# Optimization experiments

Hardware: AMD Instinct MI355X
Metric: run time of the kernel (lower is better)

## Reference

```python
import jax, jax.numpy as jnp
import numpy as np

B, S, E = 8, 2048, 256
NQ = 10
FF = 1024


def _cnot(state, c, t, n):
    # state: [T, 2^n]; wire 0 is the most-significant bit.
    T = state.shape[0]
    s = state.reshape((T,) + (2,) * n)
    ctrl0 = jnp.take(s, 0, axis=c + 1)
    ctrl1 = jnp.take(s, 1, axis=c + 1)
    # target axis index after removing the control axis
    t_ax = t + 1 if (t + 1) < (c + 1) else t
    ctrl1 = jnp.flip(ctrl1, axis=t_ax)  # X on target where control==1
    s = jnp.stack([ctrl0, ctrl1], axis=c + 1)
    return s.reshape(T, -1)


def _quantum_layer(tok, theta, n):
    # tok: [T, E] real; uses first n features as RX angles. Returns [T, n] PauliZ expvals.
    T = tok.shape[0]
    half = tok[:, :n] * 0.5
    c = jnp.cos(half).astype(jnp.complex64)
    s = (-1j * jnp.sin(half)).astype(jnp.complex64)
    # RX(theta)|0> = cos(t/2)|0> - i sin(t/2)|1>; build product state wire-by-wire
    state = jnp.ones((T, 1), dtype=jnp.complex64)
    for w in range(n):
        qb = jnp.stack([c[:, w], s[:, w]], axis=1)  # [T, 2]
        state = (state[:, :, None] * qb[:, None, :]).reshape(T, -1)
    # trainable RY per wire
    th = theta * 0.5
    for w in range(n):
        ct, st = jnp.cos(th[w]), jnp.sin(th[w])
        U = jnp.stack([jnp.stack([ct, -st]), jnp.stack([st, ct])]).astype(jnp.complex64)
        sr = state.reshape(T, 2 ** w, 2, -1)
        state = jnp.einsum('ij,tajb->taib', U, sr).reshape(T, -1)
    # CNOT ring
    for cw in range(n - 1):
        state = _cnot(state, cw, cw + 1, n)
    state = _cnot(state, n - 1, 0, n)
    probs = state.real ** 2 + state.imag ** 2  # [T, 2^n]
    idx = jnp.arange(2 ** n)
    bits = (idx[None, :] >> (n - 1 - jnp.arange(n)[:, None])) & 1  # [n, 2^n]
    z = (1.0 - 2.0 * bits).astype(probs.dtype)
    return probs @ z.T  # [T, n]


def setup_inputs() -> dict:
    key = jax.random.key(0)
    ks = jax.random.split(key, 6)
    return {
        'x': jax.random.normal(ks[0], (B, S, E), dtype=jnp.float32),
        'theta': jax.random.normal(ks[1], (NQ,), dtype=jnp.float32),
        'w1': jax.random.normal(ks[2], (FF, NQ), dtype=jnp.float32) * (1.0 / np.sqrt(NQ)),
        'b1': jax.random.normal(ks[3], (FF,), dtype=jnp.float32) * 0.02,
        'w2': jax.random.normal(ks[4], (E, FF), dtype=jnp.float32) * (1.0 / np.sqrt(FF)),
        'b2': jax.random.normal(ks[5], (E,), dtype=jnp.float32) * 0.02,
    }


def reference(x, theta, w1, b1, w2, b2):
    b, s, e = x.shape
    n = theta.shape[0]
    q = _quantum_layer(x.reshape(b * s, e), theta, n).reshape(b, s, n)
    # dropout is identity in eval mode
    h = jax.nn.relu(q @ w1.T + b1)
    return h @ w2.T + b2
```

## Files before the change

### kernel.cpp

```cpp
#include <hip/hip_runtime.h>
#include <hip/hip_bf16.h>
#include <math.h>

typedef __attribute__((ext_vector_type(8))) short bf16x8;
typedef __attribute__((ext_vector_type(4))) float f32x4;

#define T_TOT 16384
#define E_ 256
#define FF_ 1024
#define NQ 10
#define TB 64
#define CH 256
#define NCHUNK (FF_ / CH)
#define HGRAN (TB * CH)

__device__ __forceinline__ unsigned pkbf(float a, float b) {
    __hip_bfloat162 t = __float22bfloat162_rn(make_float2(a, b));
    return *(unsigned*)&t;
}

__global__ __launch_bounds__(256) void ffq_prep(
    const float* __restrict__ w2, const float* __restrict__ w1,
    uint4* __restrict__ w2f, uint4* __restrict__ w1f)
{
    int id = blockIdx.x * 256 + threadIdx.x;
    if (id < 32768) {
        int n  = id >> 7;
        int k0 = (id & 127) * 8;
        const float4* s = (const float4*)(w2 + (size_t)n * FF_ + k0);
        float4 a = s[0], b = s[1];
        uint4 v;
        v.x = pkbf(a.x, a.y);
        v.y = pkbf(a.z, a.w);
        v.z = pkbf(b.x, b.y);
        v.w = pkbf(b.z, b.w);
        int idx = ((k0 >> 5) * 16 + (n >> 4)) * 64 + ((k0 >> 3) & 3) * 16 + (n & 15);
        w2f[idx] = v;
    } else if (id < 32768 + 4096) {
        int id2 = id - 32768;
        int l = id2 & 63, nt = id2 >> 6;
        int n = nt * 16 + (l & 15);
        int g = l >> 4;
        float o[8];
#pragma unroll
        for (int j = 0; j < 8; ++j) {
            int k = g * 8 + j;
            o[j] = (k < NQ) ? w1[n * NQ + k] : 0.f;
        }
        uint4 v;
        v.x = pkbf(o[0], o[1]);
        v.y = pkbf(o[2], o[3]);
        v.z = pkbf(o[4], o[5]);
        v.w = pkbf(o[6], o[7]);
        w1f[id2] = v;
    }
}

__global__ __launch_bounds__(512, 4) void ffq_mfma(
    const float* __restrict__ x, const float* __restrict__ theta,
    const float* __restrict__ b1, const float* __restrict__ b2,
    const bf16x8* __restrict__ w1f, const bf16x8* __restrict__ w2f,
    float* __restrict__ out)
{
    __shared__ unsigned short q_s[4 * 64 * 8];
    __shared__ unsigned short hs[2 * HGRAN];

    const int tid  = threadIdx.x;
    const int l    = tid & 63;
    const int wv   = tid >> 6;
    const int lr   = l & 15;
    const int g    = l >> 4;
    const int wk   = wv >> 2;
    const int wc   = wv & 3;
    const int chb  = blockIdx.x & 1;
    const int tb   = (blockIdx.x >> 1) * TB;
    const int nc0  = chb * 8 + wc * 2;
    const int nc1  = nc0 + 1;

    if (tid < TB) {
        const int t = tb + tid;
        float xv[NQ];
        {
            float4 a = *(const float4*)(x + (size_t)t * E_);
            float4 b = *(const float4*)(x + (size_t)t * E_ + 4);
            float2 c = *(const float2*)(x + (size_t)t * E_ + 8);
            xv[0]=a.x; xv[1]=a.y; xv[2]=a.z; xv[3]=a.w;
            xv[4]=b.x; xv[5]=b.y; xv[6]=b.z; xv[7]=b.w;
            xv[8]=c.x; xv[9]=c.y;
        }
        float mm[NQ];
#pragma unroll
        for (int w = 0; w < NQ; ++w) mm[w] = cosf(theta[w]) * cosf(xv[w]);
        float qv[NQ];
        {
            float p = mm[0];
#pragma unroll
            for (int w = 1; w < NQ; ++w) { p *= mm[w]; qv[w] = p; }
            float p0 = mm[1];
#pragma unroll
            for (int w = 2; w < NQ; ++w) p0 *= mm[w];
            qv[0] = p0;
        }
        uint4 s0, s1;
        s0.x = pkbf(qv[0], qv[1]);
        s0.y = pkbf(qv[2], qv[3]);
        s0.z = pkbf(qv[4], qv[5]);
        s0.w = pkbf(qv[6], qv[7]);
        s1.x = pkbf(qv[8], qv[9]);
        s1.y = 0; s1.z = 0; s1.w = 0;
        int tt = tid >> 4, r = tid & 15;
        uint4* base = (uint4*)q_s + tt * 64;
        base[r]      = s0;
        base[16 + r] = s1;
        base[32 + r] = make_uint4(0, 0, 0, 0);
        base[48 + r] = make_uint4(0, 0, 0, 0);
    }
    __syncthreads();

    f32x4 acc[4][2];
#pragma unroll
    for (int tt = 0; tt < 4; ++tt)
#pragma unroll
        for (int nn = 0; nn < 2; ++nn) acc[tt][nn] = (f32x4){0.f,0.f,0.f,0.f};

#define H_PHASE(cc, hdst)                                                      \
    {                                                                          \
        bf16x8 wfa = w1f[((cc) * 16 + wv * 2 + 0) * 64 + l];                   \
        bf16x8 wfb = w1f[((cc) * 16 + wv * 2 + 1) * 64 + l];                   \
        float4 bba = *(const float4*)(b1 + ((cc) * 16 + wv * 2 + 0) * 16 + g * 4); \
        float4 bbb = *(const float4*)(b1 + ((cc) * 16 + wv * 2 + 1) * 16 + g * 4); \
        bf16x8 qfr[4];                                                         \
        _Pragma("unroll")                                                      \
        for (int tt = 0; tt < 4; ++tt)                                         \
            qfr[tt] = ((const bf16x8*)q_s)[tt * 64 + l];                       \
        _Pragma("unroll")                                                      \
        for (int fi = 0; fi < 2; ++fi) {                                       \
            const int ftl = wv * 2 + fi;                                       \
            bf16x8 wf = fi ? wfb : wfa;                                        \
            float4 bb = fi ? bbb : bba;                                        \
            const int fl   = ftl * 16 + g * 4;                                 \
            const int sl   = (fl & 31) >> 3;                                   \
            const int gran = (fl >> 5) * 64 + lr + 16 * sl;                    \
            _Pragma("unroll")                                                  \
            for (int tt = 0; tt < 4; ++tt) {                                   \
                f32x4 d = {0.f, 0.f, 0.f, 0.f};                                \
                d = __builtin_amdgcn_mfma_f32_16x16x32_bf16(                   \
                        wf, qfr[tt], d, 0, 0, 0);                              \
                unsigned p0 = pkbf(fmaxf(d[0] + bb.x, 0.f),                    \
                                   fmaxf(d[1] + bb.y, 0.f));                   \
                unsigned p1 = pkbf(fmaxf(d[2] + bb.z, 0.f),                    \
                                   fmaxf(d[3] + bb.w, 0.f));                   \
                unsigned byteoff = (unsigned)(tt * 512 + gran) * 16u           \
                                 + (unsigned)(fl & 7) * 2u;                    \
                *(uint2*)((char*)(hdst) + byteoff) = make_uint2(p0, p1);       \
            }                                                                  \
        }                                                                      \
    }

#define OUT_STEP(J)                                                            \
    {                                                                          \
        const int kk  = c * 8 + wk * 4 + (J);                                  \
        const int kkn = ((J) < 3) ? kk + 1 : ((c < NCHUNK - 1) ? kk + 5 : kk); \
        bf16x8 af[4];                                                          \
        _Pragma("unroll")                                                      \
        for (int tt = 0; tt < 4; ++tt)                                         \
            af[tt] = hc[(tt * 8 + wk * 4 + (J)) * 64 + l];                     \
        bf16x8 bn0 = w2f[(kkn * 16 + nc0) * 64 + l];                           \
        bf16x8 bn1 = w2f[(kkn * 16 + nc1) * 64 + l];                           \
        _Pragma("unroll")                                                      \
        for (int tt = 0; tt < 4; ++tt)                                         \
            acc[tt][0] = __builtin_amdgcn_mfma_f32_16x16x32_bf16(              \
                af[tt], bc0, acc[tt][0], 0, 0, 0);                             \
        _Pragma("unroll")                                                      \
        for (int tt = 0; tt < 4; ++tt)                                         \
            acc[tt][1] = __builtin_amdgcn_mfma_f32_16x16x32_bf16(              \
                af[tt], bc1, acc[tt][1], 0, 0, 0);                             \
        bc0 = bn0; bc1 = bn1;                                                  \
    }

    H_PHASE(0, hs)
    bf16x8 bc0 = w2f[((wk * 4) * 16 + nc0) * 64 + l];
    bf16x8 bc1 = w2f[((wk * 4) * 16 + nc1) * 64 + l];
    __syncthreads();

    for (int c = 0; c < NCHUNK; ++c) {
        const bf16x8*   hc = (const bf16x8*)(hs + (c & 1) * HGRAN);
        unsigned short* hn = hs + ((c & 1) ^ 1) * HGRAN;

        __builtin_amdgcn_s_setprio(1);
        OUT_STEP(0)
        OUT_STEP(1)
        OUT_STEP(2)
        OUT_STEP(3)
        __builtin_amdgcn_s_setprio(0);

        if (c < NCHUNK - 1) {
            H_PHASE(c + 1, hn)
        }
        __syncthreads();
    }
#undef OUT_STEP
#undef H_PHASE

    float* pbuf = (float*)hs;
    const int idx = wc * 64 + l;
    if (wk == 1) {
#pragma unroll
        for (int tt = 0; tt < 4; ++tt) {
            *(f32x4*)&pbuf[idx * 36 + tt * 8]     = acc[tt][0];
            *(f32x4*)&pbuf[idx * 36 + tt * 8 + 4] = acc[tt][1];
        }
    }
    __syncthreads();
    if (wk == 0) {
#pragma unroll
        for (int tt = 0; tt < 4; ++tt) {
            f32x4 p0 = *(const f32x4*)&pbuf[idx * 36 + tt * 8];
            f32x4 p1 = *(const f32x4*)&pbuf[idx * 36 + tt * 8 + 4];
#pragma unroll
            for (int r = 0; r < 4; ++r) { acc[tt][0][r] += p0[r]; acc[tt][1][r] += p1[r]; }
        }

#pragma unroll
        for (int nn = 0; nn < 2; ++nn) {
            const int col = (nc0 + nn) * 16 + lr;
            const float bbv = b2[col];
#pragma unroll
            for (int tt = 0; tt < 4; ++tt) {
#pragma unroll
                for (int r = 0; r < 4; ++r) {
                    int tr = tb + tt * 16 + g * 4 + r;
                    out[(size_t)tr * E_ + col] = acc[tt][nn][r] + bbv;
                }
            }
        }
    }
}

extern "C" void kernel_launch(void* const* d_in, const int* in_sizes, int n_in,
                              void* d_out, int out_size, void* d_ws, size_t ws_size,
                              hipStream_t stream) {
    const float* x     = (const float*)d_in[0];
    const float* theta = (const float*)d_in[1];
    const float* w1    = (const float*)d_in[2];
    const float* b1    = (const float*)d_in[3];
    const float* w2    = (const float*)d_in[4];
    const float* b2    = (const float*)d_in[5];
    float* out = (float*)d_out;

    uint4* w2f = (uint4*)d_ws;
    uint4* w1f = (uint4*)((char*)d_ws + 512 * 1024);

    hipLaunchKernelGGL(ffq_prep, dim3(144), dim3(256), 0, stream,
                       w2, w1, w2f, w1f);
    hipLaunchKernelGGL(ffq_mfma, dim3(2 * T_TOT / TB), dim3(512), 0, stream,
                       x, theta, b1, b2,
                       (const bf16x8*)w1f, (const bf16x8*)w2f, out);
}
```

Before: 26.20 us.

## Fuse weight bf16 conversion into main kernel, drop separate prep launch

```diff
diff --git a/kernel.cpp b/kernel.cpp
--- a/kernel.cpp
+++ b/kernel.cpp
@@ -18,48 +18,17 @@
     __hip_bfloat162 t = __float22bfloat162_rn(make_float2(a, b));
     return *(unsigned*)&t;
 }
-
-__global__ __launch_bounds__(256) void ffq_prep(
-    const float* __restrict__ w2, const float* __restrict__ w1,
-    uint4* __restrict__ w2f, uint4* __restrict__ w1f)
-{
-    int id = blockIdx.x * 256 + threadIdx.x;
-    if (id < 32768) {
-        int n  = id >> 7;
-        int k0 = (id & 127) * 8;
-        const float4* s = (const float4*)(w2 + (size_t)n * FF_ + k0);
-        float4 a = s[0], b = s[1];
-        uint4 v;
-        v.x = pkbf(a.x, a.y);
-        v.y = pkbf(a.z, a.w);
-        v.z = pkbf(b.x, b.y);
-        v.w = pkbf(b.z, b.w);
-        int idx = ((k0 >> 5) * 16 + (n >> 4)) * 64 + ((k0 >> 3) & 3) * 16 + (n & 15);
-        w2f[idx] = v;
-    } else if (id < 32768 + 4096) {
-        int id2 = id - 32768;
-        int l = id2 & 63, nt = id2 >> 6;
-        int n = nt * 16 + (l & 15);
-        int g = l >> 4;
-        float o[8];
-#pragma unroll
-        for (int j = 0; j < 8; ++j) {
-            int k = g * 8 + j;
-            o[j] = (k < NQ) ? w1[n * NQ + k] : 0.f;
-        }
-        uint4 v;
-        v.x = pkbf(o[0], o[1]);
-        v.y = pkbf(o[2], o[3]);
-        v.z = pkbf(o[4], o[5]);
-        v.w = pkbf(o[6], o[7]);
-        w1f[id2] = v;
-    }
-}
-
-__global__ __launch_bounds__(512, 4) void ffq_mfma(
+__device__ __forceinline__ bf16x8 cvt8(float4 a, float4 b) {
+    uint4 v;
+    v.x = pkbf(a.x, a.y); v.y = pkbf(a.z, a.w);
+    v.z = pkbf(b.x, b.y); v.w = pkbf(b.z, b.w);
+    return __builtin_bit_cast(bf16x8, v);
+}
+
+__global__ __launch_bounds__(512, 4) void ffq_fused(
     const float* __restrict__ x, const float* __restrict__ theta,
-    const float* __restrict__ b1, const float* __restrict__ b2,
-    const bf16x8* __restrict__ w1f, const bf16x8* __restrict__ w2f,
+    const float* __restrict__ w1, const float* __restrict__ b1,
+    const float* __restrict__ w2, const float* __restrict__ b2,
     float* __restrict__ out)
 {
     __shared__ unsigned short q_s[4 * 64 * 8];
@@ -76,6 +45,9 @@
     const int tb   = (blockIdx.x >> 1) * TB;
     const int nc0  = chb * 8 + wc * 2;
     const int nc1  = nc0 + 1;
+
+    const float* w2p0 = w2 + (size_t)(nc0 * 16 + lr) * FF_ + g * 8;
+    const float* w2p1 = w2 + (size_t)(nc1 * 16 + lr) * FF_ + g * 8;
 
     if (tid < TB) {
         const int t = tb + tid;
@@ -125,8 +97,25 @@
 
 #define H_PHASE(cc, hdst)                                                      \
     {                                                                          \
-        bf16x8 wfa = w1f[((cc) * 16 + wv * 2 + 0) * 64 + l];                   \
-        bf16x8 wfb = w1f[((cc) * 16 + wv * 2 + 1) * 64 + l];                   \
+        bf16x8 wfv[2];                                                         \
+        _Pragma("unroll")                                                      \
+        for (int fi = 0; fi < 2; ++fi) {                                       \
+            const int ntg = (cc) * 16 + wv * 2 + fi;                           \
+            const float* row = w1 + (size_t)(ntg * 16 + lr) * NQ;              \
+            float4 wa = {0.f,0.f,0.f,0.f}, wb = {0.f,0.f,0.f,0.f};             \
+            if (g == 0) {                                                      \
+                float2 p0 = *(const float2*)(row + 0);                         \
+                float2 p1 = *(const float2*)(row + 2);                         \
+                float2 p2 = *(const float2*)(row + 4);                         \
+                float2 p3 = *(const float2*)(row + 6);                         \
+                wa = make_float4(p0.x, p0.y, p1.x, p1.y);                      \
+                wb = make_float4(p2.x, p2.y, p3.x, p3.y);                      \
+            } else if (g == 1) {                                               \
+                float2 p0 = *(const float2*)(row + 8);                         \
+                wa.x = p0.x; wa.y = p0.y;                                      \
+            }                                                                  \
+            wfv[fi] = cvt8(wa, wb);                                            \
+        }                                                                      \
         float4 bba = *(const float4*)(b1 + ((cc) * 16 + wv * 2 + 0) * 16 + g * 4); \
         float4 bbb = *(const float4*)(b1 + ((cc) * 16 + wv * 2 + 1) * 16 + g * 4); \
         bf16x8 qfr[4];                                                         \
@@ -136,7 +125,6 @@
         _Pragma("unroll")                                                      \
         for (int fi = 0; fi < 2; ++fi) {                                       \
             const int ftl = wv * 2 + fi;                                       \
-            bf16x8 wf = fi ? wfb : wfa;                                        \
             float4 bb = fi ? bbb : bba;                                        \
             const int fl   = ftl * 16 + g * 4;                                 \
             const int sl   = (fl & 31) >> 3;                                   \
@@ -145,7 +133,7 @@
             for (int tt = 0; tt < 4; ++tt) {                                   \
                 f32x4 d = {0.f, 0.f, 0.f, 0.f};                                \
                 d = __builtin_amdgcn_mfma_f32_16x16x32_bf16(                   \
-                        wf, qfr[tt], d, 0, 0, 0);                              \
+                        wfv[fi], qfr[tt], d, 0, 0, 0);                         \
                 unsigned p0 = pkbf(fmaxf(d[0] + bb.x, 0.f),                    \
                                    fmaxf(d[1] + bb.y, 0.f));                   \
                 unsigned p1 = pkbf(fmaxf(d[2] + bb.z, 0.f),                    \
@@ -161,12 +149,16 @@
     {                                                                          \
         const int kk  = c * 8 + wk * 4 + (J);                                  \
         const int kkn = ((J) < 3) ? kk + 1 : ((c < NCHUNK - 1) ? kk + 5 : kk); \
+        bf16x8 bc0 = cvt8(br0a, br0b);                                         \
+        bf16x8 bc1 = cvt8(br1a, br1b);                                         \
+        br0a = *(const float4*)(w2p0 + kkn * 32);                              \
+        br0b = *(const float4*)(w2p0 + kkn * 32 + 4);                          \
+        br1a = *(const float4*)(w2p1 + kkn * 32);                              \
+        br1b = *(const float4*)(w2p1 + kkn * 32 + 4);                          \
         bf16x8 af[4];                                                          \
         _Pragma("unroll")                                                      \
         for (int tt = 0; tt < 4; ++tt)                                         \
             af[tt] = hc[(tt * 8 + wk * 4 + (J)) * 64 + l];                     \
-        bf16x8 bn0 = w2f[(kkn * 16 + nc0) * 64 + l];                           \
-        bf16x8 bn1 = w2f[(kkn * 16 + nc1) * 64 + l];                           \
         _Pragma("unroll")                                                      \
         for (int tt = 0; tt < 4; ++tt)                                         \
             acc[tt][0] = __builtin_amdgcn_mfma_f32_16x16x32_bf16(              \
@@ -175,12 +167,13 @@
         for (int tt = 0; tt < 4; ++tt)                                         \
             acc[tt][1] = __builtin_amdgcn_mfma_f32_16x16x32_bf16(              \
                 af[tt], bc1, acc[tt][1], 0, 0, 0);                             \
-        bc0 = bn0; bc1 = bn1;                                                  \
     }
 
     H_PHASE(0, hs)
-    bf16x8 bc0 = w2f[((wk * 4) * 16 + nc0) * 64 + l];
-    bf16x8 bc1 = w2f[((wk * 4) * 16 + nc1) * 64 + l];
+    float4 br0a = *(const float4*)(w2p0 + (wk * 4) * 32);
+    float4 br0b = *(const float4*)(w2p0 + (wk * 4) * 32 + 4);
+    float4 br1a = *(const float4*)(w2p1 + (wk * 4) * 32);
+    float4 br1b = *(const float4*)(w2p1 + (wk * 4) * 32 + 4);
     __syncthreads();
 
     for (int c = 0; c < NCHUNK; ++c) {
@@ -248,12 +241,6 @@
     const float* b2    = (const float*)d_in[5];
     float* out = (float*)d_out;
 
-    uint4* w2f = (uint4*)d_ws;
-    uint4* w1f = (uint4*)((char*)d_ws + 512 * 1024);
-
-    hipLaunchKernelGGL(ffq_prep, dim3(144), dim3(256), 0, stream,
-                       w2, w1, w2f, w1f);
-    hipLaunchKernelGGL(ffq_mfma, dim3(2 * T_TOT / TB), dim3(512), 0, stream,
-                       x, theta, b1, b2,
-                       (const bf16x8*)w1f, (const bf16x8*)w2f, out);
-}
+    hipLaunchKernelGGL(ffq_fused, dim3(2 * T_TOT / TB), dim3(512), 0, stream,
+                       x, theta, w1, b1, w2, b2, out);
+}
```

Result: slower. 43.81 us (+67.2%).

## Double token tile per block with 1024 threads and halve FF chunk size

Applied to the files above, without the earlier changes.

```diff
diff --git a/kernel.cpp b/kernel.cpp
--- a/kernel.cpp
+++ b/kernel.cpp
@@ -9,8 +9,8 @@
 #define E_ 256
 #define FF_ 1024
 #define NQ 10
-#define TB 64
-#define CH 256
+#define TB 128
+#define CH 128
 #define NCHUNK (FF_ / CH)
 #define HGRAN (TB * CH)
 
@@ -56,13 +56,13 @@
     }
 }
 
-__global__ __launch_bounds__(512, 4) void ffq_mfma(
+__global__ __launch_bounds__(1024, 4) void ffq_mfma(
     const float* __restrict__ x, const float* __restrict__ theta,
     const float* __restrict__ b1, const float* __restrict__ b2,
     const bf16x8* __restrict__ w1f, const bf16x8* __restrict__ w2f,
     float* __restrict__ out)
 {
-    __shared__ unsigned short q_s[4 * 64 * 8];
+    __shared__ unsigned short q_s[8 * 64 * 8];
     __shared__ unsigned short hs[2 * HGRAN];
 
     const int tid  = threadIdx.x;
@@ -70,8 +70,10 @@
     const int wv   = tid >> 6;
     const int lr   = l & 15;
     const int g    = l >> 4;
-    const int wk   = wv >> 2;
+    const int tg   = wv >> 3;
+    const int wk   = (wv >> 2) & 1;
     const int wc   = wv & 3;
+    const int ftl  = wv & 7;
     const int chb  = blockIdx.x & 1;
     const int tb   = (blockIdx.x >> 1) * TB;
     const int nc0  = chb * 8 + wc * 2;
@@ -123,114 +125,115 @@
 #pragma unroll
         for (int nn = 0; nn < 2; ++nn) acc[tt][nn] = (f32x4){0.f,0.f,0.f,0.f};
 
-#define H_PHASE(cc, hdst)                                                      \
+#define H_PHASE(hdst, WF, BBC)                                                 \
     {                                                                          \
-        bf16x8 wfa = w1f[((cc) * 16 + wv * 2 + 0) * 64 + l];                   \
-        bf16x8 wfb = w1f[((cc) * 16 + wv * 2 + 1) * 64 + l];                   \
-        float4 bba = *(const float4*)(b1 + ((cc) * 16 + wv * 2 + 0) * 16 + g * 4); \
-        float4 bbb = *(const float4*)(b1 + ((cc) * 16 + wv * 2 + 1) * 16 + g * 4); \
         bf16x8 qfr[4];                                                         \
         _Pragma("unroll")                                                      \
-        for (int tt = 0; tt < 4; ++tt)                                         \
-            qfr[tt] = ((const bf16x8*)q_s)[tt * 64 + l];                       \
-        _Pragma("unroll")                                                      \
-        for (int fi = 0; fi < 2; ++fi) {                                       \
-            const int ftl = wv * 2 + fi;                                       \
-            bf16x8 wf = fi ? wfb : wfa;                                        \
-            float4 bb = fi ? bbb : bba;                                        \
-            const int fl   = ftl * 16 + g * 4;                                 \
-            const int sl   = (fl & 31) >> 3;                                   \
-            const int gran = (fl >> 5) * 64 + lr + 16 * sl;                    \
-            _Pragma("unroll")                                                  \
-            for (int tt = 0; tt < 4; ++tt) {                                   \
-                f32x4 d = {0.f, 0.f, 0.f, 0.f};                                \
-                d = __builtin_amdgcn_mfma_f32_16x16x32_bf16(                   \
-                        wf, qfr[tt], d, 0, 0, 0);                              \
-                unsigned p0 = pkbf(fmaxf(d[0] + bb.x, 0.f),                    \
-                                   fmaxf(d[1] + bb.y, 0.f));                   \
-                unsigned p1 = pkbf(fmaxf(d[2] + bb.z, 0.f),                    \
-                                   fmaxf(d[3] + bb.w, 0.f));                   \
-                unsigned byteoff = (unsigned)(tt * 512 + gran) * 16u           \
-                                 + (unsigned)(fl & 7) * 2u;                    \
-                *(uint2*)((char*)(hdst) + byteoff) = make_uint2(p0, p1);       \
-            }                                                                  \
+        for (int j = 0; j < 4; ++j)                                            \
+            qfr[j] = ((const bf16x8*)q_s)[(tg * 4 + j) * 64 + l];              \
+        const int fl   = ftl * 16 + g * 4;                                     \
+        const int kkl  = fl >> 5;                                              \
+        const int sl   = (fl & 31) >> 3;                                       \
+        const int gran = kkl * 64 + lr + 16 * sl;                              \
+        _Pragma("unroll")                                                      \
+        for (int j = 0; j < 4; ++j) {                                          \
+            const int tt = tg * 4 + j;                                         \
+            f32x4 d = __builtin_amdgcn_mfma_f32_16x16x32_bf16(                 \
+                    (WF), qfr[j], (BBC), 0, 0, 0);                             \
+            unsigned p0 = pkbf(fmaxf(d[0], 0.f), fmaxf(d[1], 0.f));            \
+            unsigned p1 = pkbf(fmaxf(d[2], 0.f), fmaxf(d[3], 0.f));            \
+            unsigned byteoff = (unsigned)(tt * 256 + gran) * 16u               \
+                             + (unsigned)(fl & 7) * 2u;                        \
+            *(uint2*)((char*)(hdst) + byteoff) = make_uint2(p0, p1);           \
         }                                                                      \
     }
 
 #define OUT_STEP(J)                                                            \
     {                                                                          \
-        const int kk  = c * 8 + wk * 4 + (J);                                  \
-        const int kkn = ((J) < 3) ? kk + 1 : ((c < NCHUNK - 1) ? kk + 5 : kk); \
-        bf16x8 af[4];                                                          \
-        _Pragma("unroll")                                                      \
-        for (int tt = 0; tt < 4; ++tt)                                         \
-            af[tt] = hc[(tt * 8 + wk * 4 + (J)) * 64 + l];                     \
+        const int kk  = c * 4 + wk * 2 + (J);                                  \
+        const int kkn = ((J) == 0) ? kk + 1                                    \
+                      : ((c < NCHUNK - 1) ? kk + 3 : kk);                      \
         bf16x8 bn0 = w2f[(kkn * 16 + nc0) * 64 + l];                           \
         bf16x8 bn1 = w2f[(kkn * 16 + nc1) * 64 + l];                           \
-        _Pragma("unroll")                                                      \
-        for (int tt = 0; tt < 4; ++tt)                                         \
-            acc[tt][0] = __builtin_amdgcn_mfma_f32_16x16x32_bf16(              \
-                af[tt], bc0, acc[tt][0], 0, 0, 0);                             \
-        _Pragma("unroll")                                                      \
-        for (int tt = 0; tt < 4; ++tt)                                         \
-            acc[tt][1] = __builtin_amdgcn_mfma_f32_16x16x32_bf16(              \
-                af[tt], bc1, acc[tt][1], 0, 0, 0);                             \
+        bf16x8 af[4];                                                          \
+        _Pragma("unroll")                                                      \
+        for (int j = 0; j < 4; ++j)                                            \
+            af[j] = hc[((tg * 4 + j) * 4 + wk * 2 + (J)) * 64 + l];            \
+        _Pragma("unroll")                                                      \
+        for (int j = 0; j < 4; ++j)                                            \
+            acc[j][0] = __builtin_amdgcn_mfma_f32_16x16x32_bf16(               \
+                af[j], bc0, acc[j][0], 0, 0, 0);                               \
+        _Pragma("unroll")                                                      \
+        for (int j = 0; j < 4; ++j)                                            \
+            acc[j][1] = __builtin_amdgcn_mfma_f32_16x16x32_bf16(               \
+                af[j], bc1, acc[j][1], 0, 0, 0);                               \
         bc0 = bn0; bc1 = bn1;                                                  \
     }
 
-    H_PHASE(0, hs)
-    bf16x8 bc0 = w2f[((wk * 4) * 16 + nc0) * 64 + l];
-    bf16x8 bc1 = w2f[((wk * 4) * 16 + nc1) * 64 + l];
+    bf16x8 wfc = w1f[(0 * 8 + ftl) * 64 + l];
+    f32x4  bbc = *(const f32x4*)(b1 + (0 * 8 + ftl) * 16 + g * 4);
+    H_PHASE(hs, wfc, bbc)
+    bf16x8 bc0 = w2f[((wk * 2) * 16 + nc0) * 64 + l];
+    bf16x8 bc1 = w2f[((wk * 2) * 16 + nc1) * 64 + l];
     __syncthreads();
 
     for (int c = 0; c < NCHUNK; ++c) {
         const bf16x8*   hc = (const bf16x8*)(hs + (c & 1) * HGRAN);
         unsigned short* hn = hs + ((c & 1) ^ 1) * HGRAN;
 
+        if (c < NCHUNK - 1) {
+            wfc = w1f[((c + 1) * 8 + ftl) * 64 + l];
+            bbc = *(const f32x4*)(b1 + ((c + 1) * 8 + ftl) * 16 + g * 4);
+        }
+
         __builtin_amdgcn_s_setprio(1);
         OUT_STEP(0)
         OUT_STEP(1)
-        OUT_STEP(2)
-        OUT_STEP(3)
         __builtin_amdgcn_s_setprio(0);
 
         if (c < NCHUNK - 1) {
-            H_PHASE(c + 1, hn)
+            H_PHASE(hn, wfc, bbc)
         }
         __syncthreads();
     }
 #undef OUT_STEP
 #undef H_PHASE
 
-    float* pbuf = (float*)hs;
-    const int idx = wc * 64 + l;
+    char* pbuf = (char*)hs;
+    const int idx = (tg * 4 + wc) * 64 + l;
     if (wk == 1) {
 #pragma unroll
-        for (int tt = 0; tt < 4; ++tt) {
-            *(f32x4*)&pbuf[idx * 36 + tt * 8]     = acc[tt][0];
-            *(f32x4*)&pbuf[idx * 36 + tt * 8 + 4] = acc[tt][1];
-        }
+        for (int j = 0; j < 4; ++j)
+#pragma unroll
+            for (int nn = 0; nn < 2; ++nn) {
+                unsigned k = j * 2 + nn;
+                unsigned off = (unsigned)idx * 128u + ((k * 16u) ^ ((idx & 7) << 4));
+                *(f32x4*)(pbuf + off) = acc[j][nn];
+            }
     }
     __syncthreads();
     if (wk == 0) {
 #pragma unroll
-        for (int tt = 0; tt < 4; ++tt) {
-            f32x4 p0 = *(const f32x4*)&pbuf[idx * 36 + tt * 8];
-            f32x4 p1 = *(const f32x4*)&pbuf[idx * 36 + tt * 8 + 4];
-#pragma unroll
-            for (int r = 0; r < 4; ++r) { acc[tt][0][r] += p0[r]; acc[tt][1][r] += p1[r]; }
-        }
+        for (int j = 0; j < 4; ++j)
+#pragma unroll
+            for (int nn = 0; nn < 2; ++nn) {
+                unsigned k = j * 2 + nn;
+                unsigned off = (unsigned)idx * 128u + ((k * 16u) ^ ((idx & 7) << 4));
+                f32x4 p = *(const f32x4*)(pbuf + off);
+#pragma unroll
+                for (int r = 0; r < 4; ++r) acc[j][nn][r] += p[r];
+            }
 
 #pragma unroll
         for (int nn = 0; nn < 2; ++nn) {
             const int col = (nc0 + nn) * 16 + lr;
             const float bbv = b2[col];
 #pragma unroll
-            for (int tt = 0; tt < 4; ++tt) {
+            for (int j = 0; j < 4; ++j) {
 #pragma unroll
                 for (int r = 0; r < 4; ++r) {
-                    int tr = tb + tt * 16 + g * 4 + r;
-                    out[(size_t)tr * E_ + col] = acc[tt][nn][r] + bbv;
+                    int tr = tb + (tg * 4 + j) * 16 + g * 4 + r;
+                    out[(size_t)tr * E_ + col] = acc[j][nn][r] + bbv;
                 }
             }
         }
@@ -253,7 +256,7 @@
 
     hipLaunchKernelGGL(ffq_prep, dim3(144), dim3(256), 0, stream,
                        w2, w1, w2f, w1f);
-    hipLaunchKernelGGL(ffq_mfma, dim3(2 * T_TOT / TB), dim3(512), 0, stream,
+    hipLaunchKernelGGL(ffq_mfma, dim3(2 * T_TOT / TB), dim3(1024), 0, stream,
                        x, theta, b1, b2,
                        (const bf16x8*)w1f, (const bf16x8*)w2f, out);
 }
```

Measured after the change: 28.16 us. +7.5%, slower.

## Split output columns across four smaller blocks and shrink hidden chunks

Applied to the files above, without the earlier changes.

```diff
diff --git a/kernel.cpp b/kernel.cpp
--- a/kernel.cpp
+++ b/kernel.cpp
@@ -10,7 +10,7 @@
 #define FF_ 1024
 #define NQ 10
 #define TB 64
-#define CH 256
+#define CH 64
 #define NCHUNK (FF_ / CH)
 #define HGRAN (TB * CH)
 
@@ -56,7 +56,7 @@
     }
 }
 
-__global__ __launch_bounds__(512, 4) void ffq_mfma(
+__global__ __launch_bounds__(256, 8) void ffq_mfma(
     const float* __restrict__ x, const float* __restrict__ theta,
     const float* __restrict__ b1, const float* __restrict__ b2,
     const bf16x8* __restrict__ w1f, const bf16x8* __restrict__ w2f,
@@ -65,17 +65,13 @@
     __shared__ unsigned short q_s[4 * 64 * 8];
     __shared__ unsigned short hs[2 * HGRAN];
 
-    const int tid  = threadIdx.x;
-    const int l    = tid & 63;
-    const int wv   = tid >> 6;
-    const int lr   = l & 15;
-    const int g    = l >> 4;
-    const int wk   = wv >> 2;
-    const int wc   = wv & 3;
-    const int chb  = blockIdx.x & 1;
-    const int tb   = (blockIdx.x >> 1) * TB;
-    const int nc0  = chb * 8 + wc * 2;
-    const int nc1  = nc0 + 1;
+    const int tid = threadIdx.x;
+    const int l   = tid & 63;
+    const int wv  = tid >> 6;
+    const int lr  = l & 15;
+    const int g   = l >> 4;
+    const int tb  = (blockIdx.x >> 2) * TB;
+    const int nc  = (blockIdx.x & 3) * 4 + wv;
 
     if (tid < TB) {
         const int t = tb + tid;
@@ -117,121 +113,88 @@
     }
     __syncthreads();
 
-    f32x4 acc[4][2];
-#pragma unroll
-    for (int tt = 0; tt < 4; ++tt)
-#pragma unroll
-        for (int nn = 0; nn < 2; ++nn) acc[tt][nn] = (f32x4){0.f,0.f,0.f,0.f};
-
-#define H_PHASE(cc, hdst)                                                      \
+    f32x4 acc[4];
+#pragma unroll
+    for (int tt = 0; tt < 4; ++tt) acc[tt] = (f32x4){0.f, 0.f, 0.f, 0.f};
+
+#define H_PHASE(cc, hdst, WF, BBC)                                             \
     {                                                                          \
-        bf16x8 wfa = w1f[((cc) * 16 + wv * 2 + 0) * 64 + l];                   \
-        bf16x8 wfb = w1f[((cc) * 16 + wv * 2 + 1) * 64 + l];                   \
-        float4 bba = *(const float4*)(b1 + ((cc) * 16 + wv * 2 + 0) * 16 + g * 4); \
-        float4 bbb = *(const float4*)(b1 + ((cc) * 16 + wv * 2 + 1) * 16 + g * 4); \
         bf16x8 qfr[4];                                                         \
         _Pragma("unroll")                                                      \
         for (int tt = 0; tt < 4; ++tt)                                         \
             qfr[tt] = ((const bf16x8*)q_s)[tt * 64 + l];                       \
-        _Pragma("unroll")                                                      \
-        for (int fi = 0; fi < 2; ++fi) {                                       \
-            const int ftl = wv * 2 + fi;                                       \
-            bf16x8 wf = fi ? wfb : wfa;                                        \
-            float4 bb = fi ? bbb : bba;                                        \
-            const int fl   = ftl * 16 + g * 4;                                 \
-            const int sl   = (fl & 31) >> 3;                                   \
-            const int gran = (fl >> 5) * 64 + lr + 16 * sl;                    \
-            _Pragma("unroll")                                                  \
-            for (int tt = 0; tt < 4; ++tt) {                                   \
-                f32x4 d = {0.f, 0.f, 0.f, 0.f};                                \
-                d = __builtin_amdgcn_mfma_f32_16x16x32_bf16(                   \
-                        wf, qfr[tt], d, 0, 0, 0);                              \
-                unsigned p0 = pkbf(fmaxf(d[0] + bb.x, 0.f),                    \
-                                   fmaxf(d[1] + bb.y, 0.f));                   \
-                unsigned p1 = pkbf(fmaxf(d[2] + bb.z, 0.f),                    \
-                                   fmaxf(d[3] + bb.w, 0.f));                   \
-                unsigned byteoff = (unsigned)(tt * 512 + gran) * 16u           \
-                                 + (unsigned)(fl & 7) * 2u;                    \
-                *(uint2*)((char*)(hdst) + byteoff) = make_uint2(p0, p1);       \
-            }                                                                  \
+        const int fl   = wv * 16 + g * 4;                \
+        const int gb   = fl >> 5;                       \
+        const int sl   = (fl & 31) >> 3;                                       \
+        const int sub  = (fl & 7) * 2;                                         \
+        _Pragma("unroll")                                                      \
+        for (int tt = 0; tt < 4; ++tt) {                                       \
+            f32x4 d = __builtin_amdgcn_mfma_f32_16x16x32_bf16(                 \
+                    (WF), qfr[tt], (BBC), 0, 0, 0);                            \
+            unsigned p0 = pkbf(fmaxf(d[0], 0.f), fmaxf(d[1], 0.f));            \
+            unsigned p1 = pkbf(fmaxf(d[2], 0.f), fmaxf(d[3], 0.f));            \
+            unsigned byteoff = (unsigned)((tt * 2 + gb) * 64 + lr + 16 * sl)   \
+                               * 16u + (unsigned)sub;                          \
+            *(uint2*)((char*)(hdst) + byteoff) = make_uint2(p0, p1);           \
         }                                                                      \
     }
 
 #define OUT_STEP(J)                                                            \
     {                                                                          \
-        const int kk  = c * 8 + wk * 4 + (J);                                  \
-        const int kkn = ((J) < 3) ? kk + 1 : ((c < NCHUNK - 1) ? kk + 5 : kk); \
+        const int kk  = c * 2 + (J);                                           \
+        const int kkn = (kk + 1 < 32) ? kk + 1 : 31;                           \
+        bf16x8 bn = w2f[(kkn * 16 + nc) * 64 + l];                             \
         bf16x8 af[4];                                                          \
         _Pragma("unroll")                                                      \
         for (int tt = 0; tt < 4; ++tt)                                         \
-            af[tt] = hc[(tt * 8 + wk * 4 + (J)) * 64 + l];                     \
-        bf16x8 bn0 = w2f[(kkn * 16 + nc0) * 64 + l];                           \
-        bf16x8 bn1 = w2f[(kkn * 16 + nc1) * 64 + l];                           \
+            af[tt] = hc[(tt * 2 + (J)) * 64 + l];                              \
         _Pragma("unroll")                                                      \
         for (int tt = 0; tt < 4; ++tt)                                         \
-            acc[tt][0] = __builtin_amdgcn_mfma_f32_16x16x32_bf16(              \
-                af[tt], bc0, acc[tt][0], 0, 0, 0);                             \
-        _Pragma("unroll")                                                      \
-        for (int tt = 0; tt < 4; ++tt)                                         \
-            acc[tt][1] = __builtin_amdgcn_mfma_f32_16x16x32_bf16(              \
-                af[tt], bc1, acc[tt][1], 0, 0, 0);                             \
-        bc0 = bn0; bc1 = bn1;                                                  \
-    }
-
-    H_PHASE(0, hs)
-    bf16x8 bc0 = w2f[((wk * 4) * 16 + nc0) * 64 + l];
-    bf16x8 bc1 = w2f[((wk * 4) * 16 + nc1) * 64 + l];
+            acc[tt] = __builtin_amdgcn_mfma_f32_16x16x32_bf16(                 \
+                af[tt], bc, acc[tt], 0, 0, 0);                                 \
+        bc = bn;                                                               \
+    }
+
+    {
+        bf16x8 wf0 = w1f[(0 * 4 + wv) * 64 + l];
+        f32x4  bb0 = *(const f32x4*)(b1 + (0 * 4 + wv) * 16 + g * 4);
+        H_PHASE(0, hs, wf0, bb0)
+    }
+    bf16x8 bc = w2f[(0 * 16 + nc) * 64 + l];
     __syncthreads();
 
     for (int c = 0; c < NCHUNK; ++c) {
         const bf16x8*   hc = (const bf16x8*)(hs + (c & 1) * HGRAN);
         unsigned short* hn = hs + ((c & 1) ^ 1) * HGRAN;
 
+        bf16x8 wfc; f32x4 bbc;
+        if (c < NCHUNK - 1) {
+            wfc = w1f[((c + 1) * 4 + wv) * 64 + l];
+            bbc = *(const f32x4*)(b1 + ((c + 1) * 4 + wv) * 16 + g * 4);
+        }
+
         __builtin_amdgcn_s_setprio(1);
         OUT_STEP(0)
         OUT_STEP(1)
-        OUT_STEP(2)
-        OUT_STEP(3)
         __builtin_amdgcn_s_setprio(0);
 
         if (c < NCHUNK - 1) {
-            H_PHASE(c + 1, hn)
+            H_PHASE(c + 1, hn, wfc, bbc)
         }
         __syncthreads();
     }
 #undef OUT_STEP
 #undef H_PHASE
 
-    float* pbuf = (float*)hs;
-    const int idx = wc * 64 + l;
-    if (wk == 1) {
+    {
+        const int col = nc * 16 + lr;
+        const float bbv = b2[col];
 #pragma unroll
         for (int tt = 0; tt < 4; ++tt) {
-            *(f32x4*)&pbuf[idx * 36 + tt * 8]     = acc[tt][0];
-            *(f32x4*)&pbuf[idx * 36 + tt * 8 + 4] = acc[tt][1];
-        }
-    }
-    __syncthreads();
-    if (wk == 0) {
-#pragma unroll
-        for (int tt = 0; tt < 4; ++tt) {
-            f32x4 p0 = *(const f32x4*)&pbuf[idx * 36 + tt * 8];
-            f32x4 p1 = *(const f32x4*)&pbuf[idx * 36 + tt * 8 + 4];
-#pragma unroll
-            for (int r = 0; r < 4; ++r) { acc[tt][0][r] += p0[r]; acc[tt][1][r] += p1[r]; }
-        }
-
-#pragma unroll
-        for (int nn = 0; nn < 2; ++nn) {
-            const int col = (nc0 + nn) * 16 + lr;
-            const float bbv = b2[col];
-#pragma unroll
-            for (int tt = 0; tt < 4; ++tt) {
-#pragma unroll
-                for (int r = 0; r < 4; ++r) {
-                    int tr = tb + tt * 16 + g * 4 + r;
-                    out[(size_t)tr * E_ + col] = acc[tt][nn][r] + bbv;
-                }
+#pragma unroll
+            for (int r = 0; r < 4; ++r) {
+                int tr = tb + tt * 16 + g * 4 + r;
+                out[(size_t)tr * E_ + col] = acc[tt][r] + bbv;
             }
         }
     }
@@ -253,7 +216,7 @@
 
     hipLaunchKernelGGL(ffq_prep, dim3(144), dim3(256), 0, stream,
                        w2, w1, w2f, w1f);
-    hipLaunchKernelGGL(ffq_mfma, dim3(2 * T_TOT / TB), dim3(512), 0, stream,
+    hipLaunchKernelGGL(ffq_mfma, dim3(4 * T_TOT / TB), dim3(256), 0, stream,
                        x, theta, b1, b2,
                        (const bf16x8*)w1f, (const bf16x8*)w2f, out);
 }
```

Result: slower. 30.69 us (+17.1%).
